# Performance work log

Hardware: AMD Instinct MI355X
Metric: run time of the kernel (lower is better)

Reference implementation:

```python
import jax, jax.numpy as jnp
import numpy as np

T, B, H, I = 128, 32, 256, 256


def setup_inputs() -> dict:
    key = jax.random.key(0)
    ks = jax.random.split(key, 8)
    s = 0.05
    embs = jax.random.normal(ks[0], (T, B, I), jnp.float32)
    lens = jax.random.randint(ks[1], (B,), 1, T + 1)  # lengths in [1, T]
    W_ih = jax.random.normal(ks[2], (4 * H, I), jnp.float32) * s
    W_hh = jax.random.normal(ks[3], (4 * H, H), jnp.float32) * s
    b_ih = jax.random.normal(ks[4], (4 * H,), jnp.float32) * s
    b_hh = jax.random.normal(ks[5], (4 * H,), jnp.float32) * s
    W_a = jax.random.normal(ks[6], (H, 2 * H), jnp.float32) * s  # attention combine (Luong-style)
    b_a = jax.random.normal(ks[7], (H,), jnp.float32) * s
    return {"embs": embs, "lens": lens, "W_ih": W_ih, "W_hh": W_hh,
            "b_ih": b_ih, "b_hh": b_hh, "W_a": W_a, "b_a": b_a}


def reference(embs, lens, W_ih, W_hh, b_ih, b_hh, W_a, b_a):
    Tn, Bn, _ = embs.shape
    Hn = W_hh.shape[1]
    t_idx = jnp.arange(Tn)

    def step(carry, inp):
        h, c, buf, h_fin, c_fin = carry  # h,c: [B,H]; buf: [T,B,H] history of outputs
        t, emb = inp
        # dot-product attention of current hidden over past outputs (steps < t)
        scores = jnp.einsum('tbh,bh->tb', buf, h)
        valid = (t_idx < t)[:, None]
        alpha = jax.nn.softmax(jnp.where(valid, scores, -1e9), axis=0)
        ctx = jnp.einsum('tb,tbh->bh', alpha, buf)
        h_att = jnp.tanh(jnp.concatenate([ctx, h], axis=-1) @ W_a.T + b_a)
        h = jnp.where(t > 0, h_att, h)  # no history at t=0
        # standard PyTorch LSTM cell (gate order i,f,g,o)
        gates = emb @ W_ih.T + b_ih + h @ W_hh.T + b_hh
        i_g, f_g, g_g, o_g = jnp.split(gates, 4, axis=-1)
        c = jax.nn.sigmoid(f_g) * c + jax.nn.sigmoid(i_g) * jnp.tanh(g_g)
        h = jax.nn.sigmoid(o_g) * jnp.tanh(c)
        buf = buf.at[t].set(h)
        take = (t == lens - 1)[:, None]
        h_fin = jnp.where(take, h, h_fin)
        c_fin = jnp.where(take, c, c_fin)
        return (h, c, buf, h_fin, c_fin), h

    z = jnp.zeros((Bn, Hn), embs.dtype)
    buf0 = jnp.zeros((Tn, Bn, Hn), embs.dtype)
    carry, output = jax.lax.scan(step, (z, z, buf0, z, z), (t_idx, embs))
    # output: [T,B,H]; final (h,c) gathered at t == lens-1: [B,H]
    return output, carry[3], carry[4]
```

## Files before the change

kernel.cpp:

```cpp
#include <hip/hip_runtime.h>


#define T_DIM 128
#define B_DIM 32

typedef _Float16 half2_t __attribute__((ext_vector_type(2)));

static __device__ __forceinline__ unsigned pack2(float a, float b) {
  half2_t h;
  h.x = (_Float16)a;
  h.y = (_Float16)b;
  return __builtin_bit_cast(unsigned, h);
}

static __device__ __forceinline__ float dot2f(unsigned w, unsigned v, float acc) {
  half2_t a = __builtin_bit_cast(half2_t, w);
  half2_t b = __builtin_bit_cast(half2_t, v);
#if __has_builtin(__builtin_amdgcn_fdot2)
  return __builtin_amdgcn_fdot2(a, b, acc, false);
#else
  return acc + (float)a.x * (float)b.x + (float)a.y * (float)b.y;
#endif
}

static __device__ __forceinline__ float dot8(uint4 w, uint4 v, float acc) {
  acc = dot2f(w.x, v.x, acc);
  acc = dot2f(w.y, v.y, acc);
  acc = dot2f(w.z, v.z, acc);
  acc = dot2f(w.w, v.w, acc);
  return acc;
}

static __device__ __forceinline__ float lo16(unsigned u) {
  return (float)__builtin_bit_cast(half2_t, u).x;
}
static __device__ __forceinline__ float hi16(unsigned u) {
  return (float)__builtin_bit_cast(half2_t, u).y;
}

__global__ void pack_weights(const float* __restrict__ W_ih, const float* __restrict__ W_hh,
                             const float* __restrict__ W_a, float* __restrict__ W_ihT,
                             uint4* __restrict__ Whh_pack, uint4* __restrict__ Wa_pack,
                             unsigned* __restrict__ zbuf) {
  int n = blockIdx.x * 256 + threadIdx.x;
  {
    int k = n >> 10, r = n & 1023;
    W_ihT[n] = W_ih[r * 256 + k];
  }
  if (n < 32768) {
    int m = n >> 12, tid = (n >> 3) & 511, i = n & 7;
    int r_local = tid >> 2, qk = tid & 3;
    int q = r_local >> 5, jl = r_local & 31;
    int r = q * 256 + m * 32 + jl;
    const float* src = W_hh + r * 256 + (4 * i + qk) * 8;
    uint4 v;
    v.x = pack2(src[0], src[1]);
    v.y = pack2(src[2], src[3]);
    v.z = pack2(src[4], src[5]);
    v.w = pack2(src[6], src[7]);
    Whh_pack[n] = v;
  }
  if (n < 16384) {
    int m = n >> 11, tid = (n >> 2) & 511, i = n & 3;
    int j = m * 32 + (tid >> 4), part = tid & 15;
    int col0 = (i < 2) ? (part * 16 + i * 8) : (256 + part * 16 + (i - 2) * 8);
    const float* src = W_a + j * 512 + col0;
    uint4 v;
    v.x = pack2(src[0], src[1]);
    v.y = pack2(src[2], src[3]);
    v.z = pack2(src[4], src[5]);
    v.w = pack2(src[6], src[7]);
    Wa_pack[n] = v;
  }
  if (n < 24576) zbuf[n] = 0u;
}

__global__ void compute_gih(const float* __restrict__ embs, const float* __restrict__ W_ihT,
                            const float* __restrict__ b_ih, const float* __restrict__ b_hh,
                            float* __restrict__ gih) {
  __shared__ float embS[8][256];
  const int tid = threadIdx.x;
  const int tb0 = blockIdx.x * 8;
#pragma unroll
  for (int e = 0; e < 8; ++e) embS[e][tid] = embs[(size_t)(tb0 + e) * 256 + tid];
  __syncthreads();
  float acc[8][4];
#pragma unroll
  for (int e = 0; e < 8; ++e)
#pragma unroll
    for (int q = 0; q < 4; ++q) acc[e][q] = 0.f;
  for (int k = 0; k < 256; ++k) {
    float w0 = W_ihT[k * 1024 + tid];
    float w1 = W_ihT[k * 1024 + tid + 256];
    float w2 = W_ihT[k * 1024 + tid + 512];
    float w3 = W_ihT[k * 1024 + tid + 768];
#pragma unroll
    for (int e = 0; e < 8; ++e) {
      float x = embS[e][k];
      acc[e][0] += x * w0;
      acc[e][1] += x * w1;
      acc[e][2] += x * w2;
      acc[e][3] += x * w3;
    }
  }
#pragma unroll
  for (int q = 0; q < 4; ++q) {
    float bias = b_ih[q * 256 + tid] + b_hh[q * 256 + tid];
#pragma unroll
    for (int e = 0; e < 8; ++e)
      gih[(size_t)(tb0 + e) * 1024 + q * 256 + tid] = acc[e][q] + bias;
  }
}

__global__ void __launch_bounds__(512, 1)
alstm_rec(const int* __restrict__ lens, const float* __restrict__ gih,
          const uint4* __restrict__ Whh_pack, const uint4* __restrict__ Wa_pack,
          const float* __restrict__ b_a, unsigned long long* __restrict__ hx,
          unsigned long long* __restrict__ ywx, float* __restrict__ out,
          float* __restrict__ hfin, float* __restrict__ cfin) {
  const int tid = threadIdx.x;
  const int b = blockIdx.x & 31;
  const int m = blockIdx.x >> 5;

  __shared__ __align__(16) unsigned histS[16384];
  __shared__ __align__(16) unsigned ystoreS[16384];
  __shared__ __align__(16) unsigned h2[128];
  __shared__ __align__(16) unsigned hp2[128];
  __shared__ float sc[128];
  __shared__ float zpartF[4][256];
  __shared__ float gsl[128];

  uint4 wh4[8];
  {
    const uint4* p = Whh_pack + ((size_t)m * 512 + tid) * 8;
#pragma unroll
    for (int i = 0; i < 8; ++i) wh4[i] = p[i];
  }
  uint4 wa4[4];
  {
    const uint4* p = Wa_pack + ((size_t)m * 512 + tid) * 4;
#pragma unroll
    for (int i = 0; i < 4; ++i) wa4[i] = p[i];
  }
  const float ba_j = (tid < 256) ? b_a[tid] : 0.f;
  const int len_b = lens[b];
  const int r_local = tid >> 2, qk = tid & 3;
  const int gq = r_local >> 5, gjl = r_local & 31;
  const int part_a = tid & 15;

  if (tid < 128) hp2[tid] = 0u;
  float c_reg = 0.f;
  __syncthreads();

  for (int t = 0; t < T_DIM; ++t) {
    float gih_v = gih[((size_t)t * 32 + b) * 1024 + gq * 256 + m * 32 + gjl];

    float w_j = 0.f;
    if (t > 0) {
      {
        uint4 hc0 = *(const uint4*)&h2[part_a * 8];
        uint4 hc1 = *(const uint4*)&h2[part_a * 8 + 4];
        float ay = dot8(wa4[0], hc0, 0.f);
        ay = dot8(wa4[1], hc1, ay);
        float aw = dot8(wa4[2], hc0, 0.f);
        aw = dot8(wa4[3], hc1, aw);
        ay += __shfl_xor(ay, 1);
        ay += __shfl_xor(ay, 2);
        ay += __shfl_xor(ay, 4);
        ay += __shfl_xor(ay, 8);
        aw += __shfl_xor(aw, 1);
        aw += __shfl_xor(aw, 2);
        aw += __shfl_xor(aw, 4);
        aw += __shfl_xor(aw, 8);
        if (part_a == 0) {
          unsigned long long v =
              ((unsigned long long)pack2(ay, aw) << 32) | (unsigned long long)(unsigned)t;
          __hip_atomic_store(&ywx[b * 256 + m * 32 + (tid >> 4)], v, __ATOMIC_RELAXED,
                             __HIP_MEMORY_SCOPE_AGENT);
        }
      }
      {
        const int s = tid >> 2, part = tid & 3;
        float a = 0.f;
        if (s < t) {
          const int sx = s & 31;
#pragma unroll
          for (int i = 0; i < 8; ++i) {
            const int c = 4 * i + part;
            uint4 hv = *(const uint4*)&histS[s * 128 + ((c ^ sx) << 2)];
            uint4 qv = *(const uint4*)&h2[c << 2];
            a = dot8(hv, qv, a);
          }
        }
        a += __shfl_xor(a, 1);
        a += __shfl_xor(a, 2);
        if (part == 0 && s < t) sc[s] = a;
      }
      __syncthreads();
      if (tid < 64) {
        float v0 = (tid < t) ? sc[tid] : -3.0e38f;
        float v1 = (tid + 64 < t) ? sc[tid + 64] : -3.0e38f;
        float mx = fmaxf(v0, v1);
#pragma unroll
        for (int off = 32; off >= 1; off >>= 1) mx = fmaxf(mx, __shfl_xor(mx, off));
        float e0 = (tid < t) ? __expf(v0 - mx) : 0.f;
        float e1 = (tid + 64 < t) ? __expf(v1 - mx) : 0.f;
        float sm = e0 + e1;
#pragma unroll
        for (int off = 32; off >= 1; off >>= 1) sm += __shfl_xor(sm, off);
        float inv = 1.f / sm;
        sc[tid] = e0 * inv;
        sc[tid + 64] = e1 * inv;
      }
      __syncthreads();
      if (tid < 256) {
        unsigned long long v;
        for (;;) {
          v = __hip_atomic_load(&ywx[b * 256 + tid], __ATOMIC_RELAXED, __HIP_MEMORY_SCOPE_AGENT);
          if ((unsigned)v == (unsigned)t) break;
          __builtin_amdgcn_s_sleep(1);
        }
        unsigned py = (unsigned)(v >> 32);
        w_j = hi16(py);
        unsigned ny = (unsigned)__shfl_xor((int)py, 1);
        if (!(tid & 1)) {
          unsigned pair = (py & 0xFFFFu) | (ny << 16);
          const int p = tid >> 1, sx = (t - 1) & 31;
          ystoreS[(t - 1) * 128 + ((((p >> 2) ^ sx) << 2) | (p & 3))] = pair;
        }
      }
      __syncthreads();
      {
        const int sp = tid >> 7, p2 = tid & 127;
        float c0 = 0.f, c1 = 0.f;
        for (int s = sp; s < t; s += 4) {
          float al = sc[s];
          unsigned yv = ystoreS[s * 128 + ((((p2 >> 2) ^ (s & 31)) << 2) | (p2 & 3))];
          c0 += al * lo16(yv);
          c1 += al * hi16(yv);
        }
        zpartF[sp][2 * p2] = c0;
        zpartF[sp][2 * p2 + 1] = c1;
      }
      __syncthreads();
      if (tid < 256) {
        float z = zpartF[0][tid] + zpartF[1][tid] + zpartF[2][tid] + zpartF[3][tid];
        float hv = tanhf(ba_j + w_j + z);
        float o = __shfl_xor(hv, 1);
        if (!(tid & 1)) hp2[tid >> 1] = pack2(hv, o);
      }
      __syncthreads();
    }
    {
      float a = 0.f;
#pragma unroll
      for (int i = 0; i < 8; ++i) {
        const int c = 4 * i + qk;
        uint4 hv = *(const uint4*)&hp2[c << 2];
        a = dot8(wh4[i], hv, a);
      }
      a += __shfl_xor(a, 1);
      a += __shfl_xor(a, 2);
      if (qk == 0) gsl[r_local] = a + gih_v;
    }
    __syncthreads();
    if (tid < 32) {
      float ig = 1.f / (1.f + __expf(-gsl[tid]));
      float fg = 1.f / (1.f + __expf(-gsl[32 + tid]));
      float gg = tanhf(gsl[64 + tid]);
      float og = 1.f / (1.f + __expf(-gsl[96 + tid]));
      float cn = fg * c_reg + ig * gg;
      float hn = og * tanhf(cn);
      c_reg = cn;
      out[((size_t)t * 32 + b) * 256 + m * 32 + tid] = hn;
      if (t == len_b - 1) {
        hfin[b * 256 + m * 32 + tid] = hn;
        cfin[b * 256 + m * 32 + tid] = cn;
      }
      float o = __shfl_xor(hn, 1);
      if (!(tid & 1)) {
        unsigned long long v =
            ((unsigned long long)pack2(hn, o) << 32) | (unsigned long long)(unsigned)(t + 1);
        __hip_atomic_store(&hx[b * 128 + m * 16 + (tid >> 1)], v, __ATOMIC_RELAXED,
                           __HIP_MEMORY_SCOPE_AGENT);
      }
    }
    if (tid < 128) {
      const unsigned want = (unsigned)(t + 1);
      unsigned long long v;
      for (;;) {
        v = __hip_atomic_load(&hx[b * 128 + tid], __ATOMIC_RELAXED, __HIP_MEMORY_SCOPE_AGENT);
        if ((unsigned)v == want) break;
        __builtin_amdgcn_s_sleep(1);
      }
      unsigned pair = (unsigned)(v >> 32);
      h2[tid] = pair;
      histS[t * 128 + ((((tid >> 2) ^ (t & 31)) << 2) | (tid & 3))] = pair;
    }
    __syncthreads();
  }
}

extern "C" void kernel_launch(void* const* d_in, const int* in_sizes, int n_in,
                              void* d_out, int out_size, void* d_ws, size_t ws_size,
                              hipStream_t stream) {
  const float* embs = (const float*)d_in[0];
  const int* lens = (const int*)d_in[1];
  const float* W_ih = (const float*)d_in[2];
  const float* W_hh = (const float*)d_in[3];
  const float* b_ih = (const float*)d_in[4];
  const float* b_hh = (const float*)d_in[5];
  const float* W_a = (const float*)d_in[6];
  const float* b_a = (const float*)d_in[7];

  float* out = (float*)d_out;
  float* hfin = out + (size_t)T_DIM * B_DIM * 256;
  float* cfin = hfin + (size_t)B_DIM * 256;

  char* ws = (char*)d_ws;
  float* gih = (float*)ws;
  float* W_ihT = (float*)(ws + 16777216);
  uint4* Whh_pack = (uint4*)(ws + 17825792);
  uint4* Wa_pack = (uint4*)(ws + 18350080);
  unsigned long long* hx = (unsigned long long*)(ws + 18612224);
  unsigned long long* ywx = (unsigned long long*)(ws + 18644992);

  pack_weights<<<1024, 256, 0, stream>>>(W_ih, W_hh, W_a, W_ihT, Whh_pack, Wa_pack,
                                         (unsigned*)hx);
  compute_gih<<<512, 256, 0, stream>>>(embs, W_ihT, b_ih, b_hh, gih);
  alstm_rec<<<256, 512, 0, stream>>>(lens, gih, Whh_pack, Wa_pack, b_a, hx, ywx, out, hfin,
                                     cfin);
}
```

Measured before the change: 633.4 us.

## Exchange partial W_a projections so each block computes from its own h slice

The attention projection W_a·[h] is now split by input columns rather than output rows. Each block multiplies its freshly computed 32-element h slice by its W_a columns and publishes partial y/w sums to a per-batch buffer of 8 partials. Consumers poll and sum these 8 partials, and the wait for h and the wait for the projections are merged into one phase at the start of the next step, which removes one cross-block sync round per step. The change also swaps tanhf, the sigmoid and the softmax division for exp/rcp-based fast approximations, which may slightly lower accuracy.

```diff
diff --git a/kernel.cpp b/kernel.cpp
--- a/kernel.cpp
+++ b/kernel.cpp
@@ -38,10 +38,19 @@
   return (float)__builtin_bit_cast(half2_t, u).y;
 }
 
+static __device__ __forceinline__ float fsig(float x) {
+  return __builtin_amdgcn_rcpf(1.f + __expf(-x));
+}
+static __device__ __forceinline__ float ftanh(float x) {
+  float e = __expf(2.f * x);
+  return 1.f - 2.f * __builtin_amdgcn_rcpf(e + 1.f);
+}
+
 __global__ void pack_weights(const float* __restrict__ W_ih, const float* __restrict__ W_hh,
                              const float* __restrict__ W_a, float* __restrict__ W_ihT,
                              uint4* __restrict__ Whh_pack, uint4* __restrict__ Wa_pack,
-                             unsigned* __restrict__ zbuf) {
+                             unsigned long long* __restrict__ ywp,
+                             unsigned long long* __restrict__ hx) {
   int n = blockIdx.x * 256 + threadIdx.x;
   {
     int k = n >> 10, r = n & 1023;
@@ -61,9 +70,9 @@
     Whh_pack[n] = v;
   }
   if (n < 16384) {
-    int m = n >> 11, tid = (n >> 2) & 511, i = n & 3;
-    int j = m * 32 + (tid >> 4), part = tid & 15;
-    int col0 = (i < 2) ? (part * 16 + i * 8) : (256 + part * 16 + (i - 2) * 8);
+    int m = n >> 11, thr = (n >> 2) & 511, c = n & 3;
+    int j = thr >> 1, type = thr & 1;
+    int col0 = type * 256 + m * 32 + c * 8;
     const float* src = W_a + j * 512 + col0;
     uint4 v;
     v.x = pack2(src[0], src[1]);
@@ -72,7 +81,10 @@
     v.w = pack2(src[6], src[7]);
     Wa_pack[n] = v;
   }
-  if (n < 24576) zbuf[n] = 0u;
+  if (n < 65536)
+    __hip_atomic_store(&ywp[n], 0ull, __ATOMIC_RELAXED, __HIP_MEMORY_SCOPE_AGENT);
+  else if (n < 69632)
+    __hip_atomic_store(&hx[n - 65536], 0ull, __ATOMIC_RELAXED, __HIP_MEMORY_SCOPE_AGENT);
 }
 
 __global__ void compute_gih(const float* __restrict__ embs, const float* __restrict__ W_ihT,
@@ -116,7 +128,7 @@
 alstm_rec(const int* __restrict__ lens, const float* __restrict__ gih,
           const uint4* __restrict__ Whh_pack, const uint4* __restrict__ Wa_pack,
           const float* __restrict__ b_a, unsigned long long* __restrict__ hx,
-          unsigned long long* __restrict__ ywx, float* __restrict__ out,
+          unsigned long long* __restrict__ ywp, float* __restrict__ out,
           float* __restrict__ hfin, float* __restrict__ cfin) {
   const int tid = threadIdx.x;
   const int b = blockIdx.x & 31;
@@ -126,6 +138,7 @@
   __shared__ __align__(16) unsigned ystoreS[16384];
   __shared__ __align__(16) unsigned h2[128];
   __shared__ __align__(16) unsigned hp2[128];
+  __shared__ __align__(16) unsigned hsl2[16];
   __shared__ float sc[128];
   __shared__ float zpartF[4][256];
   __shared__ float gsl[128];
@@ -146,7 +159,6 @@
   const int len_b = lens[b];
   const int r_local = tid >> 2, qk = tid & 3;
   const int gq = r_local >> 5, gjl = r_local & 31;
-  const int part_a = tid & 15;
 
   if (tid < 128) hp2[tid] = 0u;
   float c_reg = 0.f;
@@ -154,31 +166,48 @@
 
   for (int t = 0; t < T_DIM; ++t) {
     float gih_v = gih[((size_t)t * 32 + b) * 1024 + gq * 256 + m * 32 + gjl];
-
     float w_j = 0.f;
+
     if (t > 0) {
-      {
-        uint4 hc0 = *(const uint4*)&h2[part_a * 8];
-        uint4 hc1 = *(const uint4*)&h2[part_a * 8 + 4];
-        float ay = dot8(wa4[0], hc0, 0.f);
-        ay = dot8(wa4[1], hc1, ay);
-        float aw = dot8(wa4[2], hc0, 0.f);
-        aw = dot8(wa4[3], hc1, aw);
-        ay += __shfl_xor(ay, 1);
-        ay += __shfl_xor(ay, 2);
-        ay += __shfl_xor(ay, 4);
-        ay += __shfl_xor(ay, 8);
-        aw += __shfl_xor(aw, 1);
-        aw += __shfl_xor(aw, 2);
-        aw += __shfl_xor(aw, 4);
-        aw += __shfl_xor(aw, 8);
-        if (part_a == 0) {
-          unsigned long long v =
-              ((unsigned long long)pack2(ay, aw) << 32) | (unsigned long long)(unsigned)t;
-          __hip_atomic_store(&ywx[b * 256 + m * 32 + (tid >> 4)], v, __ATOMIC_RELAXED,
-                             __HIP_MEMORY_SCOPE_AGENT);
-        }
-      }
+      if (tid < 256) {
+        const unsigned long long* base = ywp + b * 2048 + tid;
+        unsigned long long v[8];
+        for (;;) {
+          bool ok = true;
+#pragma unroll
+          for (int mm = 0; mm < 8; ++mm)
+            v[mm] = __hip_atomic_load(base + mm * 256, __ATOMIC_RELAXED, __HIP_MEMORY_SCOPE_AGENT);
+#pragma unroll
+          for (int mm = 0; mm < 8; ++mm) ok &= ((unsigned)v[mm] == (unsigned)t);
+          if (ok) break;
+          __builtin_amdgcn_s_sleep(1);
+        }
+        float y = 0.f, w = 0.f;
+#pragma unroll
+        for (int mm = 0; mm < 8; ++mm) {
+          unsigned pl = (unsigned)(v[mm] >> 32);
+          y += lo16(pl);
+          w += hi16(pl);
+        }
+        w_j = w;
+        float yn = __shfl_xor(y, 1);
+        if (!(tid & 1)) {
+          const int p = tid >> 1, sx = (t - 1) & 31;
+          ystoreS[(t - 1) * 128 + ((((p >> 2) ^ sx) << 2) | (p & 3))] = pack2(y, yn);
+        }
+      } else if (tid < 384) {
+        const int p = tid - 256;
+        unsigned long long v;
+        for (;;) {
+          v = __hip_atomic_load(&hx[b * 128 + p], __ATOMIC_RELAXED, __HIP_MEMORY_SCOPE_AGENT);
+          if ((unsigned)v == (unsigned)t) break;
+          __builtin_amdgcn_s_sleep(1);
+        }
+        unsigned pair = (unsigned)(v >> 32);
+        h2[p] = pair;
+        histS[(t - 1) * 128 + ((((p >> 2) ^ ((t - 1) & 31)) << 2) | (p & 3))] = pair;
+      }
+      __syncthreads();
       {
         const int s = tid >> 2, part = tid & 3;
         float a = 0.f;
@@ -208,26 +237,9 @@
         float sm = e0 + e1;
 #pragma unroll
         for (int off = 32; off >= 1; off >>= 1) sm += __shfl_xor(sm, off);
-        float inv = 1.f / sm;
+        float inv = __builtin_amdgcn_rcpf(sm);
         sc[tid] = e0 * inv;
         sc[tid + 64] = e1 * inv;
-      }
-      __syncthreads();
-      if (tid < 256) {
-        unsigned long long v;
-        for (;;) {
-          v = __hip_atomic_load(&ywx[b * 256 + tid], __ATOMIC_RELAXED, __HIP_MEMORY_SCOPE_AGENT);
-          if ((unsigned)v == (unsigned)t) break;
-          __builtin_amdgcn_s_sleep(1);
-        }
-        unsigned py = (unsigned)(v >> 32);
-        w_j = hi16(py);
-        unsigned ny = (unsigned)__shfl_xor((int)py, 1);
-        if (!(tid & 1)) {
-          unsigned pair = (py & 0xFFFFu) | (ny << 16);
-          const int p = tid >> 1, sx = (t - 1) & 31;
-          ystoreS[(t - 1) * 128 + ((((p >> 2) ^ sx) << 2) | (p & 3))] = pair;
-        }
       }
       __syncthreads();
       {
@@ -245,7 +257,7 @@
       __syncthreads();
       if (tid < 256) {
         float z = zpartF[0][tid] + zpartF[1][tid] + zpartF[2][tid] + zpartF[3][tid];
-        float hv = tanhf(ba_j + w_j + z);
+        float hv = ftanh(ba_j + w_j + z);
         float o = __shfl_xor(hv, 1);
         if (!(tid & 1)) hp2[tid >> 1] = pack2(hv, o);
       }
@@ -265,12 +277,12 @@
     }
     __syncthreads();
     if (tid < 32) {
-      float ig = 1.f / (1.f + __expf(-gsl[tid]));
-      float fg = 1.f / (1.f + __expf(-gsl[32 + tid]));
-      float gg = tanhf(gsl[64 + tid]);
-      float og = 1.f / (1.f + __expf(-gsl[96 + tid]));
+      float ig = fsig(gsl[tid]);
+      float fg = fsig(gsl[32 + tid]);
+      float gg = ftanh(gsl[64 + tid]);
+      float og = fsig(gsl[96 + tid]);
       float cn = fg * c_reg + ig * gg;
-      float hn = og * tanhf(cn);
+      float hn = og * ftanh(cn);
       c_reg = cn;
       out[((size_t)t * 32 + b) * 256 + m * 32 + tid] = hn;
       if (t == len_b - 1) {
@@ -279,25 +291,30 @@
       }
       float o = __shfl_xor(hn, 1);
       if (!(tid & 1)) {
+        unsigned u = pack2(hn, o);
+        hsl2[tid >> 1] = u;
         unsigned long long v =
-            ((unsigned long long)pack2(hn, o) << 32) | (unsigned long long)(unsigned)(t + 1);
+            ((unsigned long long)u << 32) | (unsigned long long)(unsigned)(t + 1);
         __hip_atomic_store(&hx[b * 128 + m * 16 + (tid >> 1)], v, __ATOMIC_RELAXED,
                            __HIP_MEMORY_SCOPE_AGENT);
       }
     }
-    if (tid < 128) {
-      const unsigned want = (unsigned)(t + 1);
-      unsigned long long v;
-      for (;;) {
-        v = __hip_atomic_load(&hx[b * 128 + tid], __ATOMIC_RELAXED, __HIP_MEMORY_SCOPE_AGENT);
-        if ((unsigned)v == want) break;
-        __builtin_amdgcn_s_sleep(1);
-      }
-      unsigned pair = (unsigned)(v >> 32);
-      h2[tid] = pair;
-      histS[t * 128 + ((((tid >> 2) ^ (t & 31)) << 2) | (tid & 3))] = pair;
-    }
     __syncthreads();
+    {
+      float acc = 0.f;
+#pragma unroll
+      for (int c = 0; c < 4; ++c) {
+        uint4 hv = *(const uint4*)&hsl2[c * 4];
+        acc = dot8(wa4[c], hv, acc);
+      }
+      float other = __shfl_xor(acc, 1);
+      if (!(tid & 1)) {
+        unsigned long long v = ((unsigned long long)pack2(acc, other) << 32) |
+                               (unsigned long long)(unsigned)(t + 1);
+        __hip_atomic_store(&ywp[b * 2048 + m * 256 + (tid >> 1)], v, __ATOMIC_RELAXED,
+                           __HIP_MEMORY_SCOPE_AGENT);
+      }
+    }
   }
 }
 
@@ -322,12 +339,11 @@
   float* W_ihT = (float*)(ws + 16777216);
   uint4* Whh_pack = (uint4*)(ws + 17825792);
   uint4* Wa_pack = (uint4*)(ws + 18350080);
-  unsigned long long* hx = (unsigned long long*)(ws + 18612224);
-  unsigned long long* ywx = (unsigned long long*)(ws + 18644992);
-
-  pack_weights<<<1024, 256, 0, stream>>>(W_ih, W_hh, W_a, W_ihT, Whh_pack, Wa_pack,
-                                         (unsigned*)hx);
+  unsigned long long* ywp = (unsigned long long*)(ws + 18612224);
+  unsigned long long* hx = (unsigned long long*)(ws + 19136512);
+
+  pack_weights<<<1024, 256, 0, stream>>>(W_ih, W_hh, W_a, W_ihT, Whh_pack, Wa_pack, ywp, hx);
   compute_gih<<<512, 256, 0, stream>>>(embs, W_ihT, b_ih, b_hh, gih);
-  alstm_rec<<<256, 512, 0, stream>>>(lens, gih, Whh_pack, Wa_pack, b_a, hx, ywx, out, hfin,
+  alstm_rec<<<256, 512, 0, stream>>>(lens, gih, Whh_pack, Wa_pack, b_a, hx, ywp, out, hfin,
                                      cfin);
 }
```

New measurement: 623.3 us. No clear change (-1.6%).
